# Kernel optimization log

Hardware: AMD Instinct MI355X
Metric: run time of the kernel (lower is better)

## Reference

```python
import jax, jax.numpy as jnp
import numpy as np

N, C = 50000, 91
K_PRE = 1000            # pre-NMS top-k candidates (fixed shape for jit)
DET_PER_IMG = 100
SCORE_THRESH = 0.05
NMS_THRESH = 0.5
MIN_SIZE = 0.01
LOG_SCALE_CLAMP = float(np.log(1000.0 / 16.0))  # torchvision BoxCoder clamp
BBOX_W = (10.0, 10.0, 5.0, 5.0)


def setup_inputs() -> dict:
    key = jax.random.key(0)
    k1, k2, k3, k4, k5, k6 = jax.random.split(key, 6)
    class_logits = jax.random.normal(k1, (N, C), jnp.float32) * 2.0
    box_regression = jax.random.normal(k2, (N, C * 4), jnp.float32) * 0.5
    x1 = jax.random.uniform(k3, (N,), jnp.float32) * 1200.0
    y1 = jax.random.uniform(k4, (N,), jnp.float32) * 700.0
    w = jax.random.uniform(k5, (N,), jnp.float32) * 150.0 + 4.0
    h = jax.random.uniform(k6, (N,), jnp.float32) * 150.0 + 4.0
    proposals = jnp.stack([x1, y1, x1 + w, y1 + h], axis=1)
    return {"class_logits": class_logits, "box_regression": box_regression,
            "proposals": proposals, "image_h": 800, "image_w": 1333}


def _decode(rel, props):
    # torchvision BoxCoder.decode_single with weights (10,10,5,5)
    wx, wy, ww, wh = BBOX_W
    pw = props[:, 2] - props[:, 0]
    ph = props[:, 3] - props[:, 1]
    cx = props[:, 0] + 0.5 * pw
    cy = props[:, 1] + 0.5 * ph
    dx = rel[:, 0] / wx
    dy = rel[:, 1] / wy
    dw = jnp.minimum(rel[:, 2] / ww, LOG_SCALE_CLAMP)
    dh = jnp.minimum(rel[:, 3] / wh, LOG_SCALE_CLAMP)
    pcx = dx * pw + cx
    pcy = dy * ph + cy
    ppw = jnp.exp(dw) * pw
    pph = jnp.exp(dh) * ph
    return jnp.stack([pcx - 0.5 * ppw, pcy - 0.5 * pph,
                      pcx + 0.5 * ppw, pcy + 0.5 * pph], axis=1)


def _iou_matrix(b):
    # b: [K,4] -> [K,K] pairwise IoU
    area = jnp.maximum(b[:, 2] - b[:, 0], 0.0) * jnp.maximum(b[:, 3] - b[:, 1], 0.0)
    lt = jnp.maximum(b[:, None, :2], b[None, :, :2])
    rb = jnp.minimum(b[:, None, 2:], b[None, :, 2:])
    wh = jnp.maximum(rb - lt, 0.0)
    inter = wh[..., 0] * wh[..., 1]
    return inter / (area[:, None] + area[None, :] - inter + 1e-7)


def _postprocess(class_logits, box_regression, proposals, image_h, image_w):
    num_classes = class_logits.shape[-1]
    n = proposals.shape[0]
    props = jnp.broadcast_to(proposals[:, None, :], (n, num_classes, 4)).reshape(-1, 4)
    boxes = _decode(box_regression.reshape(-1, 4), props)       # [N*C, 4]
    # clip_boxes_to_image
    boxes = jnp.stack([
        jnp.clip(boxes[:, 0], 0.0, float(image_w)),
        jnp.clip(boxes[:, 1], 0.0, float(image_h)),
        jnp.clip(boxes[:, 2], 0.0, float(image_w)),
        jnp.clip(boxes[:, 3], 0.0, float(image_h)),
    ], axis=1)
    scores = jax.nn.softmax(class_logits, axis=-1)               # [N, C]
    # drop background class 0
    boxes = boxes.reshape(n, num_classes, 4)[:, 1:].reshape(-1, 4)    # [N*(C-1), 4]
    scores = scores[:, 1:].reshape(-1)                                # [N*(C-1)]
    labels = jnp.broadcast_to(jnp.arange(1, num_classes), (n, num_classes - 1)).reshape(-1)
    # score threshold + remove small boxes -> mask (fixed-shape)
    w = boxes[:, 2] - boxes[:, 0]
    h = boxes[:, 3] - boxes[:, 1]
    valid = (scores > SCORE_THRESH) & (w >= MIN_SIZE) & (h >= MIN_SIZE)
    masked_scores = jnp.where(valid, scores, -1.0)
    s_k, idx = jax.lax.top_k(masked_scores, K_PRE)               # pre-NMS candidates
    b_k = boxes[idx]
    l_k = labels[idx]
    keep0 = s_k > 0.0
    # batched NMS via per-class coordinate offset
    offset = l_k.astype(b_k.dtype) * float(image_w + image_h + 2)
    iou = _iou_matrix(b_k + offset[:, None])                     # [K,K]
    ar = jnp.arange(K_PRE)
    def body(i, keep):
        sup = keep[i] & (iou[i] > NMS_THRESH) & (ar > i)
        return keep & ~sup
    keep = jax.lax.fori_loop(0, K_PRE, body, keep0)
    final_scores = jnp.where(keep, s_k, -1.0)
    s_out, j = jax.lax.top_k(final_scores, DET_PER_IMG)
    ok = s_out > 0.0
    boxes_out = jnp.where(ok[:, None], b_k[j], 0.0)
    scores_out = jnp.where(ok, s_out, 0.0)
    labels_out = jnp.where(ok, l_k[j], 0)
    return boxes_out, scores_out, labels_out


def reference(class_logits, box_regression, proposals, image_h, image_w):
    return _postprocess(class_logits, box_regression, proposals, image_h, image_w)
```

## Files before the change

kernel.cpp:

```cpp
#include <hip/hip_runtime.h>
#include <cstdint>

#define NROWS 50000
#define NCLS  91
#define KPRE  1000
#define NDET  100
#define CAP   4096
#define NBINS 512
#define BIN_OFF 7680u
#define LOGCLAMP 4.135166556742356f
#define ITERS 4
#define ROWS_PER_BLOCK 64
#define NBLK 782
#define PB 800
#define GCHUNK 128

constexpr size_t OFF_CNT     = 0;
constexpr size_t OFF_ROWMAX  = 64;
constexpr size_t OFF_COMPACT = 100096;
constexpr size_t OFF_SSCORE  = 132864;
constexpr size_t OFF_SGIDX   = 136960;
constexpr size_t OFF_SLABEL  = 141056;
constexpr size_t OFF_BRAW    = 145152;
constexpr size_t OFF_BNMS    = 161536;
constexpr size_t OFF_MASK    = 177920;
constexpr size_t OFF_PARTIAL = 305920;
constexpr size_t OFF_HIST512 = 1125120;

__device__ __forceinline__ bool decode_box(int row, int c,
    const float* __restrict__ regr, const float* __restrict__ props,
    float W, float H, float4& b) {
  const float4 rr = *reinterpret_cast<const float4*>(regr + (size_t)row * (NCLS * 4) + c * 4);
  const float4 pp = *reinterpret_cast<const float4*>(props + (size_t)row * 4);
  float pw = pp.z - pp.x, ph = pp.w - pp.y;
  float cx = pp.x + 0.5f * pw, cy = pp.y + 0.5f * ph;
  float dx = rr.x / 10.0f, dy = rr.y / 10.0f;
  float dw = fminf(rr.z / 5.0f, LOGCLAMP);
  float dh = fminf(rr.w / 5.0f, LOGCLAMP);
  float pcx = dx * pw + cx, pcy = dy * ph + cy;
  float ppw = expf(dw) * pw, pph = expf(dh) * ph;
  float x1 = fminf(fmaxf(pcx - 0.5f * ppw, 0.f), W);
  float y1 = fminf(fmaxf(pcy - 0.5f * pph, 0.f), H);
  float x2 = fminf(fmaxf(pcx + 0.5f * ppw, 0.f), W);
  float y2 = fminf(fmaxf(pcy + 0.5f * pph, 0.f), H);
  b = make_float4(x1, y1, x2, y2);
  return (x2 - x1 >= 0.01f) && (y2 - y1 >= 0.01f);
}

__global__ __launch_bounds__(256)
void pass1_kernel(const float* __restrict__ logits,
                  const float* __restrict__ regr,
                  const float* __restrict__ props,
                  const int* __restrict__ p_imh,
                  const int* __restrict__ p_imw,
                  uint16_t* __restrict__ partial,
                  uint16_t* __restrict__ rowmax) {
  __shared__ uint32_t hist[NBINS];
  const int t = threadIdx.x;
  hist[t] = 0;
  hist[t + 256] = 0;
  __syncthreads();

  const int sub  = t & 15;
  const int grp  = t >> 4;
  const int row0 = blockIdx.x * ROWS_PER_BLOCK + grp;
  const float W = (float)(*p_imw), H = (float)(*p_imh);

  float xn[6];
  {
    const int row = row0;
    const bool ok = row < NROWS;
    const float* lr = logits + (size_t)row * NCLS;
    #pragma unroll
    for (int j = 0; j < 6; ++j) {
      int c = sub + 16 * j;
      xn[j] = (ok && c < NCLS) ? lr[c] : -INFINITY;
    }
  }

  for (int it = 0; it < ITERS; ++it) {
    const int row = row0 + it * 16;
    float x[6];
    #pragma unroll
    for (int j = 0; j < 6; ++j) x[j] = xn[j];
    if (it + 1 < ITERS) {
      const int nrow = row0 + (it + 1) * 16;
      const bool ok = nrow < NROWS;
      const float* lr = logits + (size_t)nrow * NCLS;
      #pragma unroll
      for (int j = 0; j < 6; ++j) {
        int c = sub + 16 * j;
        xn[j] = (ok && c < NCLS) ? lr[c] : -INFINITY;
      }
    }
    if (row < NROWS) {
      float m = x[0];
      #pragma unroll
      for (int j = 1; j < 6; ++j) m = fmaxf(m, x[j]);
      m = fmaxf(m, __shfl_xor(m, 1));
      m = fmaxf(m, __shfl_xor(m, 2));
      m = fmaxf(m, __shfl_xor(m, 4));
      m = fmaxf(m, __shfl_xor(m, 8));
      float e[6]; float s = 0.f;
      #pragma unroll
      for (int j = 0; j < 6; ++j) {
        e[j] = (sub + 16 * j < NCLS) ? expf(x[j] - m) : 0.f;
        s += e[j];
      }
      s += __shfl_xor(s, 1);
      s += __shfl_xor(s, 2);
      s += __shfl_xor(s, 4);
      s += __shfl_xor(s, 8);

      int maxbin = 0;
      #pragma unroll
      for (int j = 0; j < 6; ++j) {
        int c = sub + 16 * j;
        if (c >= 1 && c < NCLS) {
          float score = e[j] / s;
          if (score > 0.05f) {
            float4 b;
            if (decode_box(row, c, regr, props, W, H, b)) {
              uint32_t bin = (__float_as_uint(score) >> 17) - BIN_OFF;
              atomicAdd(&hist[bin], 1u);
              if ((int)bin > maxbin) maxbin = (int)bin;
            }
          }
        }
      }
      maxbin = max(maxbin, __shfl_xor(maxbin, 1));
      maxbin = max(maxbin, __shfl_xor(maxbin, 2));
      maxbin = max(maxbin, __shfl_xor(maxbin, 4));
      maxbin = max(maxbin, __shfl_xor(maxbin, 8));
      if (sub == 0) rowmax[row] = (uint16_t)maxbin;
    }
  }
  __syncthreads();
  const int blk = blockIdx.x;
  uint32_t v0 = hist[t], v1 = hist[t + 256];
  partial[(size_t)t * PB + blk]         = (uint16_t)(v0 > 65535u ? 65535u : v0);
  partial[(size_t)(t + 256) * PB + blk] = (uint16_t)(v1 > 65535u ? 65535u : v1);
}

__global__ __launch_bounds__(64)
void binsum_kernel(const uint16_t* __restrict__ partial, uint32_t* __restrict__ hist512) {
  const int b = blockIdx.x;
  const uint32_t* r32 = reinterpret_cast<const uint32_t*>(partial + (size_t)b * PB);
  uint32_t s = 0;
  for (int k = threadIdx.x; k < NBLK / 2; k += 64) {
    uint32_t v = r32[k];
    s += (v & 0xffffu) + (v >> 16);
  }
  #pragma unroll
  for (int off = 32; off; off >>= 1) s += __shfl_xor(s, off);
  if (threadIdx.x == 0) hist512[b] = s;
}

__global__ __launch_bounds__(512)
void scan_kernel(const uint32_t* __restrict__ hist512, uint32_t* __restrict__ cnt) {
  __shared__ uint32_t sh[NBINS];
  const int t = threadIdx.x;
  uint32_t s = hist512[t];
  sh[t] = s;
  __syncthreads();
  uint32_t v = s;
  for (int off = 1; off < NBINS; off <<= 1) {
    uint32_t add = (t + off < NBINS) ? sh[t + off] : 0;
    __syncthreads();
    v += add;
    sh[t] = v;
    __syncthreads();
  }
  const uint32_t total = sh[0];
  if (total == 0) { if (t == 0) cnt[0] = 0xFFFFFFFFu; return; }
  const uint32_t target = total < (uint32_t)KPRE ? total : (uint32_t)KPRE;
  const uint32_t rs_t = sh[t];
  const uint32_t rs_n = (t < NBINS - 1) ? sh[t + 1] : 0;
  if (rs_t >= target && rs_n < target) cnt[0] = (uint32_t)t;
}

__global__ __launch_bounds__(256)
void refine_kernel(const float* __restrict__ logits,
                   const float* __restrict__ regr,
                   const float* __restrict__ props,
                   const int* __restrict__ p_imh,
                   const int* __restrict__ p_imw,
                   const uint16_t* __restrict__ rowmax,
                   uint32_t* __restrict__ cnt,
                   unsigned long long* __restrict__ compact) {
  const int t = threadIdx.x;
  const int lane = t & 63;
  const int g = lane >> 4;
  const int sub = lane & 15;
  const uint32_t cut = cnt[0];
  const int myrow0 = blockIdx.x * 256 + t;
  bool qual = (myrow0 < NROWS) && ((uint32_t)rowmax[myrow0] >= cut);
  unsigned long long bm = __ballot(qual);
  if (!bm) return;
  const int waveBase = blockIdx.x * 256 + (t & ~63);
  const float W = (float)(*p_imw), H = (float)(*p_imh);

  while (bm) {
    int bsel[4];
    #pragma unroll
    for (int k = 0; k < 4; ++k) {
      bsel[k] = bm ? (__ffsll((unsigned long long)bm) - 1) : -1;
      if (bm) bm &= bm - 1;
    }
    const int myb = bsel[g];
    const int row = waveBase + (myb >= 0 ? myb : 0);
    const float* lr = logits + (size_t)row * NCLS;

    float x[6];
    #pragma unroll
    for (int j = 0; j < 6; ++j) {
      int c = sub + 16 * j;
      x[j] = (c < NCLS) ? lr[c] : -INFINITY;
    }
    float m = x[0];
    #pragma unroll
    for (int j = 1; j < 6; ++j) m = fmaxf(m, x[j]);
    m = fmaxf(m, __shfl_xor(m, 1));
    m = fmaxf(m, __shfl_xor(m, 2));
    m = fmaxf(m, __shfl_xor(m, 4));
    m = fmaxf(m, __shfl_xor(m, 8));
    float e[6]; float s = 0.f;
    #pragma unroll
    for (int j = 0; j < 6; ++j) {
      e[j] = (sub + 16 * j < NCLS) ? expf(x[j] - m) : 0.f;
      s += e[j];
    }
    s += __shfl_xor(s, 1);
    s += __shfl_xor(s, 2);
    s += __shfl_xor(s, 4);
    s += __shfl_xor(s, 8);

    if (myb >= 0) {
      #pragma unroll
      for (int j = 0; j < 6; ++j) {
        int c = sub + 16 * j;
        if (c >= 1 && c < NCLS) {
          float score = e[j] / s;
          if (score > 0.05f) {
            float4 bb;
            if (decode_box(row, c, regr, props, W, H, bb)) {
              uint32_t bits = __float_as_uint(score);
              uint32_t bin = (bits >> 17) - BIN_OFF;
              if (bin >= cut) {
                uint32_t pos = atomicAdd(&cnt[1], 1u);
                if (pos < CAP) {
                  uint32_t gidx = (uint32_t)row * 90u + (uint32_t)(c - 1);
                  compact[pos] = ((unsigned long long)bits << 32) |
                                 (unsigned long long)(0xFFFFFFFFu - gidx);
                }
              }
            }
          }
        }
      }
    }
  }
}

__global__ __launch_bounds__(1024)
void sort_prep_kernel(const unsigned long long* __restrict__ compact,
                      const uint32_t* __restrict__ cnt,
                      const float* __restrict__ regr, const float* __restrict__ props,
                      const int* __restrict__ p_imh, const int* __restrict__ p_imw,
                      float* __restrict__ sel_score, uint32_t* __restrict__ sel_gidx,
                      int* __restrict__ slabel, float4* __restrict__ braw,
                      float4* __restrict__ bnms) {
  __shared__ unsigned long long arr[CAP];
  const int t = threadIdx.x;
  const uint32_t M = cnt[1] < (uint32_t)CAP ? cnt[1] : (uint32_t)CAP;
  int P = 1024;
  while (P < (int)M) P <<= 1;
  for (int i = t; i < P; i += 1024) arr[i] = (i < (int)M) ? compact[i] : 0ull;
  __syncthreads();
  for (int k = 2; k <= P; k <<= 1) {
    for (int j = k >> 1; j > 0; j >>= 1) {
      for (int i = t; i < P; i += 1024) {
        int l = i ^ j;
        if (l > i) {
          unsigned long long A = arr[i], B = arr[l];
          bool up = ((i & k) == 0);
          if (up ? (A > B) : (A < B)) { arr[i] = B; arr[l] = A; }
        }
      }
      __syncthreads();
    }
  }
  if (t < KPRE) {
    unsigned long long en = arr[P - 1 - t];
    float sc; uint32_t g;
    if (en) { sc = __uint_as_float((uint32_t)(en >> 32)); g = 0xFFFFFFFFu - (uint32_t)en; }
    else    { sc = -1.f; g = 0xFFFFFFFFu; }
    sel_score[t] = sc;
    sel_gidx[t] = g;
    if (sc > 0.f) {
      int row = (int)(g / 90u);
      int c   = (int)(g % 90u) + 1;
      float W = (float)(*p_imw), H = (float)(*p_imh);
      float4 b;
      decode_box(row, c, regr, props, W, H, b);
      braw[t] = b;
      float offv = (float)c * (float)(*p_imw + *p_imh + 2);
      bnms[t] = make_float4(b.x + offv, b.y + offv, b.z + offv, b.w + offv);
      slabel[t] = c;
    } else {
      braw[t] = make_float4(0, 0, 0, 0);
      bnms[t] = make_float4(0, 0, 0, 0);
      slabel[t] = 0;
    }
  }
}

__global__ __launch_bounds__(256)
void iou_kernel(const float4* __restrict__ bnms, unsigned long long* __restrict__ mask) {
  const int i = blockIdx.x;
  const int lane = threadIdx.x & 63;
  const int wv = threadIdx.x >> 6;
  const float4 bi = bnms[i];
  const float areai = fmaxf(bi.z - bi.x, 0.f) * fmaxf(bi.w - bi.y, 0.f);
  #pragma unroll
  for (int ww = 0; ww < 4; ++ww) {
    int wd = wv * 4 + ww;
    int j = wd * 64 + lane;
    bool bit = false;
    if (j < KPRE && j > i) {
      float4 bj = bnms[j];
      float areaj = fmaxf(bj.z - bj.x, 0.f) * fmaxf(bj.w - bj.y, 0.f);
      float ltx = fmaxf(bi.x, bj.x), lty = fmaxf(bi.y, bj.y);
      float rbx = fminf(bi.z, bj.z), rby = fminf(bi.w, bj.w);
      float iw = fmaxf(rbx - ltx, 0.f), ih = fmaxf(rby - lty, 0.f);
      float inter = iw * ih;
      float iou = inter / (areai + areaj - inter + 1e-7f);
      bit = iou > 0.5f;
    }
    unsigned long long mword = __ballot(bit);
    if (lane == 0) mask[(size_t)i * 16 + wd] = mword;
  }
}

__global__ __launch_bounds__(256)
void greedy_kernel(const unsigned long long* __restrict__ mask,
                   const float* __restrict__ sel_score,
                   const int* __restrict__ slabel,
                   const float4* __restrict__ braw,
                   float* __restrict__ out) {
  __shared__ ulonglong2 buf[2][GCHUNK * 8];
  __shared__ int kept[NDET];
  __shared__ int s_done;
  const int t = threadIdx.x;
  const int lane = t & 63;
  const int wv = t >> 6;
  const ulonglong2* gm2 = reinterpret_cast<const ulonglong2*>(mask);
  constexpr int NCHUNK = (KPRE + GCHUNK - 1) / GCHUNK;

  unsigned long long kw = 0ull;
  #pragma unroll
  for (int w = 0; w < 16; ++w) {
    int j = w * 64 + lane;
    bool b = (j < KPRE) && (sel_score[j] > 0.f);
    unsigned long long mword = __ballot(b);
    if (lane == w) kw = mword;
  }
  if (t == 0) s_done = 0;

  {
    int rows = (KPRE < GCHUNK) ? KPRE : GCHUNK;
    int n2 = rows * 8;
    for (int k = t; k < n2; k += 256) buf[0][k] = gm2[k];
  }
  __syncthreads();

  int kc = 0;
  for (int c = 0; c < NCHUNK; ++c) {
    if (wv > 0 && c + 1 < NCHUNK) {
      int rows = KPRE - (c + 1) * GCHUNK;
      if (rows > GCHUNK) rows = GCHUNK;
      int n2 = rows * 8;
      size_t gbase = (size_t)(c + 1) * GCHUNK * 8;
      for (int k = t - 64; k < n2; k += 192) buf[(c + 1) & 1][k] = gm2[gbase + k];
    }
    if (wv == 0) {
      const unsigned long long* bb =
          reinterpret_cast<const unsigned long long*>(buf[c & 1]);
      int rows = KPRE - c * GCHUNK;
      if (rows > GCHUNK) rows = GCHUNK;
      unsigned long long curm = (lane < 16) ? bb[lane] : 0ull;
      for (int r = 0; r < rows; ++r) {
        unsigned long long nxt =
            (lane < 16 && r + 1 < rows) ? bb[(r + 1) * 16 + lane] : 0ull;
        int i = c * GCHUNK + r;
        unsigned long long kwv = __shfl(kw, i >> 6);
        if ((kwv >> (i & 63)) & 1ull) {
          if (lane == 0) kept[kc] = i;
          kw &= ~curm;
          ++kc;
          if (kc >= NDET) { if (lane == 0) s_done = 1; break; }
        }
        curm = nxt;
      }
    }
    __syncthreads();
    if (s_done) break;
  }

  if (wv == 0) {
    for (int q = lane; q < NDET; q += 64) {
      if (q < kc) {
        int i = kept[q];
        float4 b = braw[i];
        out[q * 4 + 0] = b.x; out[q * 4 + 1] = b.y;
        out[q * 4 + 2] = b.z; out[q * 4 + 3] = b.w;
        out[4 * NDET + q] = sel_score[i];
        out[5 * NDET + q] = (float)slabel[i];
      } else {
        out[q * 4 + 0] = 0.f; out[q * 4 + 1] = 0.f;
        out[q * 4 + 2] = 0.f; out[q * 4 + 3] = 0.f;
        out[4 * NDET + q] = 0.f;
        out[5 * NDET + q] = 0.f;
      }
    }
  }
}

extern "C" void kernel_launch(void* const* d_in, const int* in_sizes, int n_in,
                              void* d_out, int out_size, void* d_ws, size_t ws_size,
                              hipStream_t stream) {
  const float* logits = (const float*)d_in[0];
  const float* regr   = (const float*)d_in[1];
  const float* props  = (const float*)d_in[2];
  const int*   p_imh  = (const int*)d_in[3];
  const int*   p_imw  = (const int*)d_in[4];
  float* out = (float*)d_out;

  uint8_t* ws = (uint8_t*)d_ws;
  uint32_t* cnt  = (uint32_t*)(ws + OFF_CNT);
  uint16_t* rowmax = (uint16_t*)(ws + OFF_ROWMAX);
  unsigned long long* compact = (unsigned long long*)(ws + OFF_COMPACT);
  float*    sel_score = (float*)(ws + OFF_SSCORE);
  uint32_t* sel_gidx  = (uint32_t*)(ws + OFF_SGIDX);
  int*      slabel    = (int*)(ws + OFF_SLABEL);
  float4*   braw      = (float4*)(ws + OFF_BRAW);
  float4*   bnms      = (float4*)(ws + OFF_BNMS);
  unsigned long long* mask = (unsigned long long*)(ws + OFF_MASK);
  uint16_t* partial   = (uint16_t*)(ws + OFF_PARTIAL);
  uint32_t* hist512   = (uint32_t*)(ws + OFF_HIST512);

  hipMemsetAsync(cnt, 0, 64, stream);

  pass1_kernel<<<NBLK, 256, 0, stream>>>(
      logits, regr, props, p_imh, p_imw, partial, rowmax);
  binsum_kernel<<<NBINS, 64, 0, stream>>>(partial, hist512);
  scan_kernel<<<1, NBINS, 0, stream>>>(hist512, cnt);
  refine_kernel<<<(NROWS + 255) / 256, 256, 0, stream>>>(
      logits, regr, props, p_imh, p_imw, rowmax, cnt, compact);
  sort_prep_kernel<<<1, 1024, 0, stream>>>(compact, cnt, regr, props, p_imh, p_imw,
                                           sel_score, sel_gidx, slabel, braw, bnms);
  iou_kernel<<<KPRE, 256, 0, stream>>>(bnms, mask);
  greedy_kernel<<<1, 256, 0, stream>>>(mask, sel_score, slabel, braw, out);
}
```

Baseline: 106.0 us.

## Use one row-group per block in pass1 and drop the memset launch

pass1 now handles 16 rows per block across 3126 blocks instead of 64 rows per block with a software-prefetched loop over 782 blocks. This gives more parallelism and removes the register-held prefetch. The partial histogram buffer grows to match, so binsum reads about four times as many per-block counts. The host memset of the counter is replaced by scan_kernel zeroing cnt[1], which removes one API call and launch. The cost is more blocks writing partial histograms, more shared-memory zeroing and a longer binsum reduction.

```diff
diff --git a/kernel.cpp b/kernel.cpp
--- a/kernel.cpp
+++ b/kernel.cpp
@@ -9,10 +9,9 @@
 #define NBINS 512
 #define BIN_OFF 7680u
 #define LOGCLAMP 4.135166556742356f
-#define ITERS 4
-#define ROWS_PER_BLOCK 64
-#define NBLK 782
-#define PB 800
+#define ROWS_PER_BLOCK 16
+#define PBLK 3126
+#define PB   3126
 #define GCHUNK 128
 
 constexpr size_t OFF_CNT     = 0;
@@ -25,7 +24,7 @@
 constexpr size_t OFF_BNMS    = 161536;
 constexpr size_t OFF_MASK    = 177920;
 constexpr size_t OFF_PARTIAL = 305920;
-constexpr size_t OFF_HIST512 = 1125120;
+constexpr size_t OFF_HIST512 = 3506944;
 
 __device__ __forceinline__ bool decode_box(int row, int c,
     const float* __restrict__ regr, const float* __restrict__ props,
@@ -61,79 +60,57 @@
   hist[t + 256] = 0;
   __syncthreads();
 
-  const int sub  = t & 15;
-  const int grp  = t >> 4;
-  const int row0 = blockIdx.x * ROWS_PER_BLOCK + grp;
-  const float W = (float)(*p_imw), H = (float)(*p_imh);
-
-  float xn[6];
-  {
-    const int row = row0;
-    const bool ok = row < NROWS;
+  const int sub = t & 15;
+  const int grp = t >> 4;
+  const int row = blockIdx.x * ROWS_PER_BLOCK + grp;
+  if (row < NROWS) {
+    const float W = (float)(*p_imw), H = (float)(*p_imh);
     const float* lr = logits + (size_t)row * NCLS;
+    float x[6];
     #pragma unroll
     for (int j = 0; j < 6; ++j) {
       int c = sub + 16 * j;
-      xn[j] = (ok && c < NCLS) ? lr[c] : -INFINITY;
-    }
-  }
-
-  for (int it = 0; it < ITERS; ++it) {
-    const int row = row0 + it * 16;
-    float x[6];
-    #pragma unroll
-    for (int j = 0; j < 6; ++j) x[j] = xn[j];
-    if (it + 1 < ITERS) {
-      const int nrow = row0 + (it + 1) * 16;
-      const bool ok = nrow < NROWS;
-      const float* lr = logits + (size_t)nrow * NCLS;
-      #pragma unroll
-      for (int j = 0; j < 6; ++j) {
-        int c = sub + 16 * j;
-        xn[j] = (ok && c < NCLS) ? lr[c] : -INFINITY;
-      }
-    }
-    if (row < NROWS) {
-      float m = x[0];
-      #pragma unroll
-      for (int j = 1; j < 6; ++j) m = fmaxf(m, x[j]);
-      m = fmaxf(m, __shfl_xor(m, 1));
-      m = fmaxf(m, __shfl_xor(m, 2));
-      m = fmaxf(m, __shfl_xor(m, 4));
-      m = fmaxf(m, __shfl_xor(m, 8));
-      float e[6]; float s = 0.f;
-      #pragma unroll
-      for (int j = 0; j < 6; ++j) {
-        e[j] = (sub + 16 * j < NCLS) ? expf(x[j] - m) : 0.f;
-        s += e[j];
-      }
-      s += __shfl_xor(s, 1);
-      s += __shfl_xor(s, 2);
-      s += __shfl_xor(s, 4);
-      s += __shfl_xor(s, 8);
-
-      int maxbin = 0;
-      #pragma unroll
-      for (int j = 0; j < 6; ++j) {
-        int c = sub + 16 * j;
-        if (c >= 1 && c < NCLS) {
-          float score = e[j] / s;
-          if (score > 0.05f) {
-            float4 b;
-            if (decode_box(row, c, regr, props, W, H, b)) {
-              uint32_t bin = (__float_as_uint(score) >> 17) - BIN_OFF;
-              atomicAdd(&hist[bin], 1u);
-              if ((int)bin > maxbin) maxbin = (int)bin;
-            }
+      x[j] = (c < NCLS) ? lr[c] : -INFINITY;
+    }
+    float m = x[0];
+    #pragma unroll
+    for (int j = 1; j < 6; ++j) m = fmaxf(m, x[j]);
+    m = fmaxf(m, __shfl_xor(m, 1));
+    m = fmaxf(m, __shfl_xor(m, 2));
+    m = fmaxf(m, __shfl_xor(m, 4));
+    m = fmaxf(m, __shfl_xor(m, 8));
+    float e[6]; float s = 0.f;
+    #pragma unroll
+    for (int j = 0; j < 6; ++j) {
+      e[j] = (sub + 16 * j < NCLS) ? expf(x[j] - m) : 0.f;
+      s += e[j];
+    }
+    s += __shfl_xor(s, 1);
+    s += __shfl_xor(s, 2);
+    s += __shfl_xor(s, 4);
+    s += __shfl_xor(s, 8);
+
+    int maxbin = 0;
+    #pragma unroll
+    for (int j = 0; j < 6; ++j) {
+      int c = sub + 16 * j;
+      if (c >= 1 && c < NCLS) {
+        float score = e[j] / s;
+        if (score > 0.05f) {
+          float4 b;
+          if (decode_box(row, c, regr, props, W, H, b)) {
+            uint32_t bin = (__float_as_uint(score) >> 17) - BIN_OFF;
+            atomicAdd(&hist[bin], 1u);
+            if ((int)bin > maxbin) maxbin = (int)bin;
           }
         }
       }
-      maxbin = max(maxbin, __shfl_xor(maxbin, 1));
-      maxbin = max(maxbin, __shfl_xor(maxbin, 2));
-      maxbin = max(maxbin, __shfl_xor(maxbin, 4));
-      maxbin = max(maxbin, __shfl_xor(maxbin, 8));
-      if (sub == 0) rowmax[row] = (uint16_t)maxbin;
-    }
+    }
+    maxbin = max(maxbin, __shfl_xor(maxbin, 1));
+    maxbin = max(maxbin, __shfl_xor(maxbin, 2));
+    maxbin = max(maxbin, __shfl_xor(maxbin, 4));
+    maxbin = max(maxbin, __shfl_xor(maxbin, 8));
+    if (sub == 0) rowmax[row] = (uint16_t)maxbin;
   }
   __syncthreads();
   const int blk = blockIdx.x;
@@ -147,7 +124,7 @@
   const int b = blockIdx.x;
   const uint32_t* r32 = reinterpret_cast<const uint32_t*>(partial + (size_t)b * PB);
   uint32_t s = 0;
-  for (int k = threadIdx.x; k < NBLK / 2; k += 64) {
+  for (int k = threadIdx.x; k < PB / 2; k += 64) {
     uint32_t v = r32[k];
     s += (v & 0xffffu) + (v >> 16);
   }
@@ -160,6 +137,7 @@
 void scan_kernel(const uint32_t* __restrict__ hist512, uint32_t* __restrict__ cnt) {
   __shared__ uint32_t sh[NBINS];
   const int t = threadIdx.x;
+  if (t == 0) cnt[1] = 0;
   uint32_t s = hist512[t];
   sh[t] = s;
   __syncthreads();
@@ -449,9 +427,8 @@
   uint16_t* partial   = (uint16_t*)(ws + OFF_PARTIAL);
   uint32_t* hist512   = (uint32_t*)(ws + OFF_HIST512);
 
-  hipMemsetAsync(cnt, 0, 64, stream);
-
-  pass1_kernel<<<NBLK, 256, 0, stream>>>(
+
+  pass1_kernel<<<PBLK, 256, 0, stream>>>(
       logits, regr, props, p_imh, p_imw, partial, rowmax);
   binsum_kernel<<<NBINS, 64, 0, stream>>>(partial, hist512);
   scan_kernel<<<1, NBINS, 0, stream>>>(hist512, cnt);
```

New measurement: 96.24 us. -9.2%, faster.
